# Optimization experiments

Measured on AMD Instinct MI355X. Metric: run time of the kernel, lower is better.

## Reference

```python
import jax, jax.numpy as jnp
import numpy as np

N_NODES = 100000
NEG_SLOPE = 0.2


def setup_inputs() -> dict:
    key = jax.random.key(0)
    k1, k2, k3, k4, k5 = jax.random.split(key, 5)
    N, E, Fin, Fout = N_NODES, 3200000, 128, 128
    x = jax.random.normal(k1, (N, Fin), dtype=jnp.float32)
    edge_index = jax.random.randint(k2, (2, E), 0, N, dtype=jnp.int64)
    # xavier-uniform for lin weight (fan_in=Fin, fan_out=Fout)
    limit = float(np.sqrt(6.0 / (Fin + Fout)))
    W = jax.random.uniform(k3, (Fin, Fout), jnp.float32, -limit, limit)
    # PyG glorot init for attention vectors (fan ~ Fout)
    alim = float(np.sqrt(6.0 / (1 + Fout)))
    att_src = jax.random.uniform(k4, (Fout,), jnp.float32, -alim, alim)
    att_dst = jax.random.uniform(k5, (Fout,), jnp.float32, -alim, alim)
    bias = jnp.zeros((Fout,), jnp.float32)
    return {"x": x, "edge_index": edge_index, "W": W,
            "att_src": att_src, "att_dst": att_dst, "bias": bias}


def reference(x, edge_index, W, att_src, att_dst, bias):
    N = x.shape[0]
    src, dst = edge_index[0], edge_index[1]  # messages flow src -> dst
    h = x @ W                                # [N, Fout]
    a_src = h @ att_src                      # [N]
    a_dst = h @ att_dst                      # [N]
    e = a_src[src] + a_dst[dst]              # [E]
    e = jax.nn.leaky_relu(e, NEG_SLOPE)
    # segment softmax over incoming edges of each dst node
    e_max = jax.ops.segment_max(e, dst, num_segments=N)  # [N]
    e_max = jnp.where(jnp.isfinite(e_max), e_max, 0.0)
    e_exp = jnp.exp(e - e_max[dst])          # [E]
    denom = jax.ops.segment_sum(e_exp, dst, num_segments=N)  # [N]
    alpha = e_exp / (denom[dst] + 1e-16)     # [E]
    # scatter-add weighted neighbor features
    out = jax.ops.segment_sum(alpha[:, None] * h[src], dst, num_segments=N)
    out = out + bias
    return jax.nn.relu(out)
```

## Files before the change

kernel.cpp:

```cpp
#include <hip/hip_runtime.h>
#include <cstdint>
#include <cstddef>

#define NEG 0.2f
#define CAP 10752
#define FINE_CAP CAP

typedef __attribute__((ext_vector_type(8))) short short8;
typedef __attribute__((ext_vector_type(4))) float f32x4;

__device__ __forceinline__ unsigned short f2bf(float f) {
  unsigned u = __float_as_uint(f);
  unsigned r = (u + 0x7fffu + ((u >> 16) & 1u)) >> 16;
  return (unsigned short)r;
}

__global__ __launch_bounds__(512) void k_detect(const int* __restrict__ ei32,
                                                int* __restrict__ flag,
                                                int* __restrict__ cursor,
                                                const float* __restrict__ W,
                                                unsigned short* __restrict__ Wt) {
  int t = threadIdx.x;
  int b = blockIdx.x;
  if (b == 0) {
    cursor[t] = t * CAP;
    if (t < 64) {
      int v = ei32[2 * t + 1];
      unsigned long long bl = __ballot(v != 0);
      if (t == 0) flag[0] = (bl == 0ULL) ? 1 : 0;
    }
  }
  int idx = b * 512 + t;
  float4 v = ((const float4*)W)[idx];
  int k = idx >> 5;
  int c = (idx & 31) * 4;
  Wt[(c + 0) * 128 + k] = f2bf(v.x);
  Wt[(c + 1) * 128 + k] = f2bf(v.y);
  Wt[(c + 2) * 128 + k] = f2bf(v.z);
  Wt[(c + 3) * 128 + k] = f2bf(v.w);
}

__device__ __forceinline__ int edge_val(const void* ei, long long idx, int is64) {
  return is64 ? (int)((const long long*)ei)[idx] : ((const int*)ei)[idx];
}

#define MS_CHUNK 4096
__global__ __launch_bounds__(256) void k_fused(
    const float* __restrict__ x, const unsigned short* __restrict__ Wt,
    const float* __restrict__ as_, const float* __restrict__ ad_,
    unsigned short* __restrict__ hb, float* __restrict__ a_s,
    float* __restrict__ a_d, int N,
    const void* __restrict__ ei, const int* __restrict__ flag,
    int* __restrict__ cursor, uint32_t* __restrict__ buck, int E, int nms) {
  __shared__ int hist[512];
  __shared__ int resv[512];
  int gid = blockIdx.x;
  int t = threadIdx.x;
  bool is_ms = ((gid % 3) == 0) && ((gid / 3) < nms);

  if (is_ms) {
    int bid = gid / 3;
    const int is64 = flag[0];
    for (int i = t; i < 512; i += 256) hist[i] = 0;
    __syncthreads();
    long long base = (long long)bid * MS_CHUNK;
    uint32_t rec[16];
    int bb[16], rk[16];
#pragma unroll
    for (int i = 0; i < 16; ++i) {
      long long idx = base + i * 256 + t;
      bb[i] = -1;
      if (idx < E) {
        int s = edge_val(ei, idx, is64);
        int d = edge_val(ei, (long long)E + idx, is64);
        bb[i] = d >> 8;
        rec[i] = ((uint32_t)(d & 255) << 17) | (uint32_t)s;
        rk[i] = atomicAdd(&hist[bb[i]], 1);
      }
    }
    __syncthreads();
    for (int b = t; b < 512; b += 256) {
      int c = hist[b];
      resv[b] = c ? atomicAdd(&cursor[b], c) : 0;
    }
    __syncthreads();
#pragma unroll
    for (int i = 0; i < 16; ++i) {
      if (bb[i] >= 0) buck[(size_t)resv[bb[i]] + rk[i]] = rec[i];
    }
    return;
  }

  int gemm_id = gid - min(gid / 3 + 1, nms);
  int lane = t & 63;
  int wv = t >> 6;
  int row0 = gemm_id * 64 + wv * 16;
  int r = lane & 15, o = lane >> 4;

  int arow = row0 + r;
  if (arow >= N) arow = N - 1;
  const float* xr = x + (size_t)arow * 128 + o * 8;
  short8 a[4];
#pragma unroll
  for (int kt = 0; kt < 4; ++kt) {
    float4 lo = *(const float4*)(xr + kt * 32);
    float4 hi = *(const float4*)(xr + kt * 32 + 4);
    short8 av;
    av[0] = (short)f2bf(lo.x); av[1] = (short)f2bf(lo.y);
    av[2] = (short)f2bf(lo.z); av[3] = (short)f2bf(lo.w);
    av[4] = (short)f2bf(hi.x); av[5] = (short)f2bf(hi.y);
    av[6] = (short)f2bf(hi.z); av[7] = (short)f2bf(hi.w);
    a[kt] = av;
  }

  float ats[8], atd[8];
#pragma unroll
  for (int ct = 0; ct < 8; ++ct) {
    ats[ct] = as_[ct * 16 + r];
    atd[ct] = ad_[ct * 16 + r];
  }

  f32x4 acc[8];
#pragma unroll
  for (int ct = 0; ct < 8; ++ct) acc[ct] = (f32x4){0.f, 0.f, 0.f, 0.f};
#pragma unroll
  for (int ct = 0; ct < 8; ++ct) {
    const unsigned short* wb = Wt + ((size_t)(ct * 16 + r)) * 128 + o * 8;
#pragma unroll
    for (int kt = 0; kt < 4; ++kt) {
      short8 b = *(const short8*)(wb + kt * 32);
      acc[ct] = __builtin_amdgcn_mfma_f32_16x16x32_bf16(a[kt], b, acc[ct], 0, 0, 0);
    }
  }

#pragma unroll
  for (int j = 0; j < 4; ++j) {
    int row = row0 + o * 4 + j;
    bool ok = row < N;
    float ps = 0.f, pd = 0.f;
#pragma unroll
    for (int ct = 0; ct < 8; ++ct) {
      float v = acc[ct][j];
      if (ok) hb[(size_t)row * 128 + ct * 16 + r] = f2bf(v);
      ps += v * ats[ct];
      pd += v * atd[ct];
    }
#pragma unroll
    for (int d = 1; d <= 8; d <<= 1) {
      ps += __shfl_xor(ps, d);
      pd += __shfl_xor(pd, d);
    }
    if (ok && r == 0) { a_s[row] = ps; a_d[row] = pd; }
  }
}

__global__ __launch_bounds__(1024) void k_fine(const int* __restrict__ cursor,
                                               const uint32_t* __restrict__ buck,
                                               int* __restrict__ offsets,
                                               uint32_t* __restrict__ fsr,
                                               int N, int E) {
  __shared__ int hist[256];
  __shared__ int cur[256];
  __shared__ int wsum8[8];
  __shared__ int wsum[4];
  __shared__ int b0_sh;
  __shared__ uint32_t stage[FINE_CAP];
  int b = blockIdx.x;
  int t = threadIdx.x;
  int lane = t & 63;
  int cnt = cursor[b] - b * CAP;
  const uint32_t* bk = buck + (size_t)b * CAP;
  int node = (b << 8) + (t & 255);

  int sv = 0, sincl = 0, sw8 = t >> 6;
  if (t < 512) {
    sv = cursor[t] - t * CAP;
    sincl = sv;
#pragma unroll
    for (int d = 1; d < 64; d <<= 1) {
      int o = __shfl_up(sincl, d);
      if (lane >= d) sincl += o;
    }
    if (lane == 63) wsum8[sw8] = sincl;
  }
  if (t < 256) hist[t] = 0;
  __syncthreads();
  if (t < 512) {
    int woff = 0;
    for (int i = 0; i < sw8; ++i) woff += wsum8[i];
    int excl = woff + sincl - sv;
    if (t == b) b0_sh = excl;
  }
  __syncthreads();
  int b0 = b0_sh;

  for (int i = t; i < cnt; i += 1024) atomicAdd(&hist[bk[i] >> 17], 1);
  __syncthreads();
  int v = 0, incl = 0;
  int w4 = t >> 6;
  if (t < 256) {
    v = hist[t];
    incl = v;
#pragma unroll
    for (int d = 1; d < 64; d <<= 1) {
      int o = __shfl_up(incl, d);
      if (lane >= d) incl += o;
    }
    if (lane == 63) wsum[w4] = incl;
  }
  __syncthreads();
  if (t < 256) {
    int woff = 0;
    for (int i = 0; i < w4; ++i) woff += wsum[i];
    int excl = woff + incl - v;
    cur[t] = excl;
    if (node < N) offsets[node] = b0 + excl;
  }
  if (b == 0 && t == 0) offsets[N] = E;
  __syncthreads();
  for (int i = t; i < cnt; i += 1024) {
    uint32_t r = bk[i];
    int pos = atomicAdd(&cur[r >> 17], 1);
    stage[pos] = r;
  }
  __syncthreads();
  for (int i = t; i < cnt; i += 1024) fsr[b0 + i] = stage[i];
}

#define AGG_LOAD(K, JJ)                                                   \
  {                                                                       \
    int e_ = ((JJ) * 4 + g) & 63;                                         \
    int ss_ = __shfl(s_l, e_);                                            \
    float ww_ = __shfl(w_l, e_);                                          \
    w##K = ((JJ) < iters) ? ww_ : 0.f;                                    \
    u##K = *(const uint4*)&hb[(size_t)ss_ * 128 + l16 * 8];               \
  }

#define AGG_FMA(K)                                                        \
  {                                                                       \
    acc[0] += w##K * __uint_as_float(u##K.x << 16);                       \
    acc[1] += w##K * __uint_as_float(u##K.x & 0xffff0000u);               \
    acc[2] += w##K * __uint_as_float(u##K.y << 16);                       \
    acc[3] += w##K * __uint_as_float(u##K.y & 0xffff0000u);               \
    acc[4] += w##K * __uint_as_float(u##K.z << 16);                       \
    acc[5] += w##K * __uint_as_float(u##K.z & 0xffff0000u);               \
    acc[6] += w##K * __uint_as_float(u##K.w << 16);                       \
    acc[7] += w##K * __uint_as_float(u##K.w & 0xffff0000u);               \
  }

__global__ __launch_bounds__(256) void k_agg(const int* __restrict__ offs,
                                             const uint32_t* __restrict__ fsr,
                                             const float* __restrict__ a_s,
                                             const float* __restrict__ a_d,
                                             const unsigned short* __restrict__ hb,
                                             const float* __restrict__ bias,
                                             float* __restrict__ out, int N) {
  int lane = threadIdx.x & 63;
  int n = blockIdx.x * 4 + (threadIdx.x >> 6);
  if (n >= N) return;
  int g = lane >> 4;
  int l16 = lane & 15;
  float acc[8] = {};
  float sum = 0.f;
  int s0 = offs[n], s1 = offs[n + 1];
  float adn = a_d[n];

  for (int base = s0; base < s1; base += 64) {
    int idx = base + lane;
    int s_l = 0;
    float w_l = 0.f;
    if (idx < s1) {
      uint32_t r = fsr[idx];
      s_l = (int)(r & 0x1ffffu);
      float e = a_s[s_l] + adn;
      e = (e > 0.f) ? e : NEG * e;
      w_l = __expf(e);
    }
    sum += w_l;
    int cnt = min(64, s1 - base);
    int iters = (cnt + 3) >> 2;
    uint4 u0, u1, u2, u3, u4;
    float w0, w1, w2, w3, w4;
    AGG_LOAD(0, 0) AGG_LOAD(1, 1) AGG_LOAD(2, 2)
    AGG_LOAD(3, 3) AGG_LOAD(4, 4)
    int j = 0;
    for (; j + 5 < iters; j += 5) {
      AGG_FMA(0) AGG_LOAD(0, j + 5)
      AGG_FMA(1) AGG_LOAD(1, j + 6)
      AGG_FMA(2) AGG_LOAD(2, j + 7)
      AGG_FMA(3) AGG_LOAD(3, j + 8)
      AGG_FMA(4) AGG_LOAD(4, j + 9)
    }
    AGG_FMA(0) AGG_FMA(1) AGG_FMA(2) AGG_FMA(3) AGG_FMA(4)
  }
#pragma unroll
  for (int d = 1; d <= 32; d <<= 1) sum += __shfl_xor(sum, d);
#pragma unroll
  for (int d = 16; d <= 32; d <<= 1) {
#pragma unroll
    for (int i = 0; i < 8; ++i) acc[i] += __shfl_xor(acc[i], d);
  }
  float inv = 1.0f / (sum + 1e-16f);
  if (lane < 32) {
    int half = g & 1;
    int f = l16 * 8 + half * 4;
    float4 bv = *(const float4*)&bias[f];
    float4 o;
    o.x = fmaxf(acc[half * 4 + 0] * inv + bv.x, 0.f);
    o.y = fmaxf(acc[half * 4 + 1] * inv + bv.y, 0.f);
    o.z = fmaxf(acc[half * 4 + 2] * inv + bv.z, 0.f);
    o.w = fmaxf(acc[half * 4 + 3] * inv + bv.w, 0.f);
    *(float4*)&out[(size_t)n * 128 + f] = o;
  }
}

extern "C" void kernel_launch(void* const* d_in, const int* in_sizes, int n_in,
                              void* d_out, int out_size, void* d_ws, size_t ws_size,
                              hipStream_t stream) {
  const float* x = (const float*)d_in[0];
  const void* ei = d_in[1];
  const float* W = (const float*)d_in[2];
  const float* att_s = (const float*)d_in[3];
  const float* att_d = (const float*)d_in[4];
  const float* bias = (const float*)d_in[5];
  float* out = (float*)d_out;

  const int N = in_sizes[0] / 128;
  const int E = in_sizes[1] / 2;
  const int NB = (N + 255) >> 8;

  uint8_t* ws = (uint8_t*)d_ws;
  size_t off = 0;
  auto alloc = [&](size_t bytes) -> void* {
    void* p = ws + off;
    off = (off + bytes + 511) & ~(size_t)511;
    return p;
  };
  int* flag = (int*)alloc(4);
  int* bcur = (int*)alloc(512 * 4);
  unsigned short* Wt = (unsigned short*)alloc(128 * 128 * 2);
  int* offsets = (int*)alloc((size_t)(N + 1) * 4);
  uint32_t* fsr = (uint32_t*)alloc((size_t)E * 4);
  unsigned short* hb = (unsigned short*)alloc((size_t)N * 128 * 2);
  float* a_s = (float*)alloc((size_t)N * 4);
  float* a_d = (float*)alloc((size_t)N * 4);
  uint32_t* buck = (uint32_t*)d_out;
  (void)ws_size; (void)n_in; (void)out_size;

  const int ngemm = (N + 63) / 64;
  const int nms = (E + MS_CHUNK - 1) / MS_CHUNK;
  int grid = ngemm + nms;
  if (grid < 3 * nms - 2) grid = 3 * nms - 2;

  k_detect<<<8, 512, 0, stream>>>((const int*)ei, flag, bcur, W, Wt);
  k_fused<<<grid, 256, 0, stream>>>(x, Wt, att_s, att_d, hb, a_s, a_d, N,
                                    ei, flag, bcur, buck, E, nms);
  k_fine<<<NB, 1024, 0, stream>>>(bcur, buck, offsets, fsr, N, E);
  k_agg<<<(N + 3) / 4, 256, 0, stream>>>(offsets, fsr, a_s, a_d, hb, bias, out, N);
}
```

Baseline: 185.1 us.

## Fuse fine bucket sort into aggregation kernel using shared-memory staging

Adds a k_aggf kernel that sorts each 256-node bucket's edges by destination in shared memory and aggregates directly from the staged list. This drops the separate k_fine launch and the global offsets/fsr round trip. The buckets move into the workspace instead of d_out so the output can be written while buckets are still being read. The cost is that each block now handles 256 nodes with only 16 waves (16 nodes per wave) and holds about 43KB of LDS, which lowers parallelism and occupancy in the aggregation phase.

```diff
diff --git a/kernel.cpp b/kernel.cpp
--- a/kernel.cpp
+++ b/kernel.cpp
@@ -314,6 +314,118 @@
   }
 }
 
+__global__ __launch_bounds__(1024) void k_aggf(const int* __restrict__ cursor,
+                                               const uint32_t* __restrict__ buck,
+                                               const float* __restrict__ a_s,
+                                               const float* __restrict__ a_d,
+                                               const unsigned short* __restrict__ hb,
+                                               const float* __restrict__ bias,
+                                               float* __restrict__ out, int N) {
+  __shared__ int hist[256];
+  __shared__ int cur[256];
+  __shared__ int excl_k[256];
+  __shared__ int wsum[4];
+  __shared__ uint32_t stage[FINE_CAP];
+  int b = blockIdx.x;
+  int t = threadIdx.x;
+  int lane = t & 63;
+  int cnt = cursor[b] - b * CAP;
+  const uint32_t* bk = buck + (size_t)b * CAP;
+
+  if (t < 256) hist[t] = 0;
+  __syncthreads();
+  for (int i = t; i < cnt; i += 1024) atomicAdd(&hist[bk[i] >> 17], 1);
+  __syncthreads();
+  int v = 0, incl = 0;
+  int w4 = t >> 6;
+  if (t < 256) {
+    v = hist[t];
+    incl = v;
+#pragma unroll
+    for (int d = 1; d < 64; d <<= 1) {
+      int o = __shfl_up(incl, d);
+      if (lane >= d) incl += o;
+    }
+    if (lane == 63) wsum[w4] = incl;
+  }
+  __syncthreads();
+  if (t < 256) {
+    int woff = 0;
+    for (int i = 0; i < w4; ++i) woff += wsum[i];
+    int excl = woff + incl - v;
+    cur[t] = excl;
+    excl_k[t] = excl;
+  }
+  __syncthreads();
+  for (int i = t; i < cnt; i += 1024) {
+    uint32_t r = bk[i];
+    int pos = atomicAdd(&cur[r >> 17], 1);
+    stage[pos] = r;
+  }
+  __syncthreads();
+
+  int wv = t >> 6;
+  int g = lane >> 4;
+  int l16 = lane & 15;
+  for (int i = 0; i < 16; ++i) {
+    int ln = wv * 16 + i;
+    int n = (b << 8) + ln;
+    if (n >= N) break;
+    int e0 = excl_k[ln];
+    int e1 = e0 + hist[ln];
+    float adn = a_d[n];
+    float acc[8] = {};
+    float sum = 0.f;
+    for (int base = e0; base < e1; base += 64) {
+      int idx = base + lane;
+      int s_l = 0;
+      float w_l = 0.f;
+      if (idx < e1) {
+        uint32_t r = stage[idx];
+        s_l = (int)(r & 0x1ffffu);
+        float e = a_s[s_l] + adn;
+        e = (e > 0.f) ? e : NEG * e;
+        w_l = __expf(e);
+      }
+      sum += w_l;
+      int cnt2 = min(64, e1 - base);
+      int iters = (cnt2 + 3) >> 2;
+      uint4 u0, u1, u2, u3, u4;
+      float w0, w1, w2, w3, w4;
+      AGG_LOAD(0, 0) AGG_LOAD(1, 1) AGG_LOAD(2, 2)
+      AGG_LOAD(3, 3) AGG_LOAD(4, 4)
+      int j = 0;
+      for (; j + 5 < iters; j += 5) {
+        AGG_FMA(0) AGG_LOAD(0, j + 5)
+        AGG_FMA(1) AGG_LOAD(1, j + 6)
+        AGG_FMA(2) AGG_LOAD(2, j + 7)
+        AGG_FMA(3) AGG_LOAD(3, j + 8)
+        AGG_FMA(4) AGG_LOAD(4, j + 9)
+      }
+      AGG_FMA(0) AGG_FMA(1) AGG_FMA(2) AGG_FMA(3) AGG_FMA(4)
+    }
+#pragma unroll
+    for (int d = 1; d <= 32; d <<= 1) sum += __shfl_xor(sum, d);
+#pragma unroll
+    for (int d = 16; d <= 32; d <<= 1) {
+#pragma unroll
+      for (int k = 0; k < 8; ++k) acc[k] += __shfl_xor(acc[k], d);
+    }
+    float inv = 1.0f / (sum + 1e-16f);
+    if (lane < 32) {
+      int half = g & 1;
+      int f = l16 * 8 + half * 4;
+      float4 bv = *(const float4*)&bias[f];
+      float4 o;
+      o.x = fmaxf(acc[half * 4 + 0] * inv + bv.x, 0.f);
+      o.y = fmaxf(acc[half * 4 + 1] * inv + bv.y, 0.f);
+      o.z = fmaxf(acc[half * 4 + 2] * inv + bv.z, 0.f);
+      o.w = fmaxf(acc[half * 4 + 3] * inv + bv.w, 0.f);
+      *(float4*)&out[(size_t)n * 128 + f] = o;
+    }
+  }
+}
+
 extern "C" void kernel_launch(void* const* d_in, const int* in_sizes, int n_in,
                               void* d_out, int out_size, void* d_ws, size_t ws_size,
                               hipStream_t stream) {
@@ -339,22 +451,33 @@
   int* flag = (int*)alloc(4);
   int* bcur = (int*)alloc(512 * 4);
   unsigned short* Wt = (unsigned short*)alloc(128 * 128 * 2);
-  int* offsets = (int*)alloc((size_t)(N + 1) * 4);
-  uint32_t* fsr = (uint32_t*)alloc((size_t)E * 4);
   unsigned short* hb = (unsigned short*)alloc((size_t)N * 128 * 2);
   float* a_s = (float*)alloc((size_t)N * 4);
   float* a_d = (float*)alloc((size_t)N * 4);
-  uint32_t* buck = (uint32_t*)d_out;
-  (void)ws_size; (void)n_in; (void)out_size;
+  (void)n_in; (void)out_size;
+
+  const size_t buck_bytes = (size_t)NB * CAP * 4;
+  const bool merged = (ws_size >= off + buck_bytes + 4096);
 
   const int ngemm = (N + 63) / 64;
   const int nms = (E + MS_CHUNK - 1) / MS_CHUNK;
   int grid = ngemm + nms;
   if (grid < 3 * nms - 2) grid = 3 * nms - 2;
 
-  k_detect<<<8, 512, 0, stream>>>((const int*)ei, flag, bcur, W, Wt);
-  k_fused<<<grid, 256, 0, stream>>>(x, Wt, att_s, att_d, hb, a_s, a_d, N,
-                                    ei, flag, bcur, buck, E, nms);
-  k_fine<<<NB, 1024, 0, stream>>>(bcur, buck, offsets, fsr, N, E);
-  k_agg<<<(N + 3) / 4, 256, 0, stream>>>(offsets, fsr, a_s, a_d, hb, bias, out, N);
-}
+  if (merged) {
+    uint32_t* buck = (uint32_t*)alloc(buck_bytes);
+    k_detect<<<8, 512, 0, stream>>>((const int*)ei, flag, bcur, W, Wt);
+    k_fused<<<grid, 256, 0, stream>>>(x, Wt, att_s, att_d, hb, a_s, a_d, N,
+                                      ei, flag, bcur, buck, E, nms);
+    k_aggf<<<NB, 1024, 0, stream>>>(bcur, buck, a_s, a_d, hb, bias, out, N);
+  } else {
+    int* offsets = (int*)alloc((size_t)(N + 1) * 4);
+    uint32_t* fsr = (uint32_t*)alloc((size_t)E * 4);
+    uint32_t* buck = (uint32_t*)d_out;
+    k_detect<<<8, 512, 0, stream>>>((const int*)ei, flag, bcur, W, Wt);
+    k_fused<<<grid, 256, 0, stream>>>(x, Wt, att_s, att_d, hb, a_s, a_d, N,
+                                      ei, flag, bcur, buck, E, nms);
+    k_fine<<<NB, 1024, 0, stream>>>(bcur, buck, offsets, fsr, N, E);
+    k_agg<<<(N + 3) / 4, 256, 0, stream>>>(offsets, fsr, a_s, a_d, hb, bias, out, N);
+  }
+}
```

Result: slower. 202.8 us (+9.5%).
